# Kernel optimization log

Hardware: AMD Instinct MI355X
Metric: run time of the kernel (lower is better)

The kernel has to match this reference:

```python
import jax, jax.numpy as jnp
import numpy as np
from jax import lax

NUM_TAGS = 54
START = 52
STOP = 53
SEQ_LEN = 512
BATCH = 1024
NEG_INF = -10000.0


def setup_inputs() -> dict:
    key = jax.random.key(0)
    k1, k2, k3 = jax.random.split(key, 3)
    emissions = jax.random.normal(k1, (SEQ_LEN, BATCH, NUM_TAGS), dtype=jnp.float32)
    transitions = jax.random.normal(k2, (NUM_TAGS, NUM_TAGS), dtype=jnp.float32)
    # __init__ clamps: cannot transition TO <start>, cannot transition FROM <stop>
    transitions = transitions.at[START, :].set(NEG_INF)
    transitions = transitions.at[:, STOP].set(NEG_INF)
    tags = jax.random.randint(k3, (SEQ_LEN, BATCH), 0, 52, dtype=jnp.int64)
    mask = jnp.ones((SEQ_LEN, BATCH), dtype=jnp.int32)
    return {"emissions": emissions, "transitions": transitions, "tags": tags, "mask": mask}


def _crf_loss(emissions, transitions, tags, mask):
    S, B, T = emissions.shape
    maskf = mask.astype(emissions.dtype)

    # ---- forward algorithm (log partition), transitions[i, j] = score(j -> i) ----
    alpha0 = jnp.full((B, T), NEG_INF, dtype=emissions.dtype).at[:, START].set(0.0)

    def step(alpha, xs):
        feat, m = xs  # feat: (B, T), m: (B,)
        # (B, T_next, T_prev)
        scores = alpha[:, None, :] + transitions[None, :, :] + feat[:, :, None]
        new_alpha = jax.scipy.special.logsumexp(scores, axis=-1)
        alpha = jnp.where(m[:, None] > 0, new_alpha, alpha)
        return alpha, None

    alpha, _ = lax.scan(step, alpha0, (emissions, maskf))
    alpha = alpha + transitions[STOP][None, :]
    forward_score = jax.scipy.special.logsumexp(alpha, axis=-1)  # (B,)

    # ---- gold score of the given tag sequence ----
    emit = jnp.take_along_axis(emissions, tags[:, :, None], axis=2)[..., 0]  # (S, B)
    trans_t = transitions[tags[1:], tags[:-1]]  # (S-1, B)
    gold = transitions[tags[0], START] + emit[0]
    gold = gold + ((trans_t + emit[1:]) * maskf[1:]).sum(axis=0)
    lengths = mask.sum(axis=0)  # (B,)
    last_tags = tags[lengths - 1, jnp.arange(B)]
    gold = gold + transitions[STOP, last_tags]

    loss = forward_score - gold  # (B,)
    # reduction == 'token_mean'
    return loss.sum() / maskf.sum()


def reference(emissions, transitions, tags, mask):
    return _crf_loss(emissions, transitions, tags, mask)
```

## Files before the change

kernel.cpp:

```cpp
#include <hip/hip_runtime.h>
#include <stdint.h>

#define SEQ    512
#define BATCH  1024
#define NTAG   54
#define TSTART 52
#define TSTOP  53
#define NW     4
#define EMROW  (BATCH * NTAG)


typedef const __attribute__((address_space(1))) void* gld_gptr;
typedef __attribute__((address_space(3))) void*       gld_lptr;

__device__ __forceinline__ void stage4(const float* g, float* l) {
    __builtin_amdgcn_global_load_lds((gld_gptr)g, (gld_lptr)l, 4, 0, 0);
}

#define STEP(o, INC) do {                                                     \
    stage4(gp, (float*)&flds[wv][((o) + 8) & 15][0]);                         \
    gp += (INC);                                                              \
    asm volatile("s_waitcnt vmcnt(8)" ::: "memory");                          \
    float fv_ = flds[wv][(o)][lane];                                          \
    alds[wv][lane] = u;                                                       \
    float efs_ = __expf(fv_) * __uint_as_float((unsigned)(127 - e_lag) << 23);\
    float a0_ = 0.f, a1_ = 0.f, a2_ = 0.f, a3_ = 0.f;                         \
    const float4* ap_ = (const float4*)(&alds[wv][0]);                        \
    _Pragma("unroll")                                                         \
    for (int g_ = 0; g_ < 14; ++g_) {                                         \
        float4 av_ = ap_[g_];                                                 \
        a0_ = fmaf(Elin[4*g_+0], av_.x, a0_);                                 \
        a1_ = fmaf(Elin[4*g_+1], av_.y, a1_);                                 \
        a2_ = fmaf(Elin[4*g_+2], av_.z, a2_);                                 \
        a3_ = fmaf(Elin[4*g_+3], av_.w, a3_);                                 \
    }                                                                         \
    float w_  = (a0_ + a1_) + (a2_ + a3_);                                    \
    float un_ = w_ * efs_;                                                    \
    bool  up_ = (cur & 1ull) != 0ull;                                         \
    cur >>= 1;                                                                \
    u = up_ ? un_ : u;                                                        \
    esum += up_ ? e_lag : 0;                                                  \
    unsigned ub_ = (unsigned)__builtin_amdgcn_readlane(__float_as_int(u), 0); \
    int en_ = (int)((ub_ >> 23) & 255u) - 127;                                \
    e_lag = en_ < -40 ? -40 : (en_ > 40 ? 40 : en_);                          \
} while (0)

__global__ __launch_bounds__(64 * NW, 1) void crf_fwd_kernel(
    const float* __restrict__ em, const float* __restrict__ tr,
    const int* __restrict__ tags, const int* __restrict__ mask,
    float* __restrict__ part, int* __restrict__ msum)
{
    __shared__ float tlds[NTAG * NTAG];
    __shared__ __align__(16) float alds[NW][64];
    __shared__ __align__(16) float flds[NW][16][64];

    const int tid = threadIdx.x;
    for (int k = tid; k < NTAG * NTAG; k += 64 * NW) tlds[k] = tr[k];
    __syncthreads();

    const int wv   = tid >> 6;
    const int lane = tid & 63;
    const int b    = blockIdx.x * NW + wv;
    const size_t bT = (size_t)b * NTAG;

    float Elin[56];
    #pragma unroll
    for (int i = 0; i < 56; ++i) {
        Elin[i] = (lane < NTAG && i < NTAG) ? __expf(tlds[lane * NTAG + i]) : 0.f;
        asm("" : "+v"(Elin[i]));
    }
    float estop = (lane < NTAG) ? __expf(tlds[TSTOP * NTAG + lane]) : 0.f;

    float    goldp = 0.f;
    int      msump = 0;
    uint64_t B[8];
    #pragma unroll
    for (int r = 0; r < 8; ++r) {
        int s  = r * 64 + lane;
        int tg = tags[s * BATCH + b];
        int mk = mask[s * BATCH + b];
        int tp = (s == 0) ? TSTART : tags[(s - 1) * BATCH + b];
        float emv = em[(size_t)s * EMROW + bT + tg];
        float trv = tlds[tg * NTAG + tp];
        float mf  = (s == 0) ? 1.f : (float)mk;
        goldp = fmaf(trv + emv, mf, goldp);
        msump += mk;
        B[r] = __ballot(mk > 0);
    }
    #pragma unroll
    for (int off = 32; off >= 1; off >>= 1) {
        goldp += __shfl_xor(goldp, off);
        msump += __shfl_xor(msump, off);
    }

    float u     = (lane == TSTART) ? 1.f : 0.f;
    int   esum  = 0;
    int   e_lag = 0;

    asm volatile("s_waitcnt vmcnt(0)" ::: "memory");

    const float* gp = em + bT + (lane < NTAG ? lane : NTAG - 1);
    #pragma unroll
    for (int s = 0; s < 8; ++s) {
        stage4(gp, (float*)&flds[wv][s][0]);
        gp += EMROW;
    }

    for (int c = 0; c < 8; ++c) {
        uint64_t cur = B[0];
        for (int q = 0; q < 4; ++q) {
            const size_t incB = (c == 7 && q == 3) ? 0 : (size_t)EMROW;
            STEP( 0, EMROW); STEP( 1, EMROW); STEP( 2, EMROW); STEP( 3, EMROW);
            STEP( 4, EMROW); STEP( 5, EMROW); STEP( 6, EMROW); STEP( 7, incB);
            STEP( 8, incB);  STEP( 9, incB);  STEP(10, incB);  STEP(11, incB);
            STEP(12, incB);  STEP(13, incB);  STEP(14, incB);  STEP(15, incB);
        }
        #pragma unroll
        for (int r = 0; r < 7; ++r) B[r] = B[r + 1];
    }

    float us = u * estop;
    #pragma unroll
    for (int off = 32; off >= 1; off >>= 1) us += __shfl_xor(us, off);
    float fwd = __logf(us) + (float)esum * 0.69314718f;

    asm volatile("s_waitcnt vmcnt(0)" ::: "memory");
    int li   = (msump > 0) ? (msump - 1) : 0;
    int ltag = tags[li * BATCH + b];
    float gold = goldp + tlds[TSTOP * NTAG + ltag];

    if (lane == 0) { part[b] = fwd - gold; msum[b] = msump; }
}

__global__ __launch_bounds__(256) void crf_reduce_kernel(
    const float* __restrict__ part, const int* __restrict__ msum,
    float* __restrict__ out)
{
    const int tid = threadIdx.x;
    float s = 0.f;
    int   m = 0;
    for (int k = tid; k < BATCH; k += 256) { s += part[k]; m += msum[k]; }
    #pragma unroll
    for (int off = 32; off >= 1; off >>= 1) {
        s += __shfl_xor(s, off);
        m += __shfl_xor(m, off);
    }
    __shared__ float sl[4];
    __shared__ int   ml[4];
    if ((tid & 63) == 0) { sl[tid >> 6] = s; ml[tid >> 6] = m; }
    __syncthreads();
    if (tid == 0)
        out[0] = (sl[0] + sl[1] + sl[2] + sl[3]) /
                 (float)(ml[0] + ml[1] + ml[2] + ml[3]);
}

extern "C" void kernel_launch(void* const* d_in, const int* in_sizes, int n_in,
                              void* d_out, int out_size, void* d_ws, size_t ws_size,
                              hipStream_t stream)
{
    const float* em   = (const float*)d_in[0];
    const float* tr   = (const float*)d_in[1];
    const int*   tags = (const int*)d_in[2];
    const int*   mask = (const int*)d_in[3];

    float* part  = (float*)d_ws;
    int*   msumw = (int*)((char*)d_ws + BATCH * sizeof(float));
    float* out   = (float*)d_out;

    crf_fwd_kernel<<<BATCH / NW, 64 * NW, 0, stream>>>(em, tr, tags, mask, part, msumw);
    crf_reduce_kernel<<<1, 256, 0, stream>>>(part, msumw, out);
}
```

Baseline: 167.4 us.

## Pack two batch sequences per wavefront with two tags per lane

Each 64-lane wavefront now handles two batch elements: each half-wave takes one sequence and every lane computes two next-tag outputs, holding two rows of exp-transitions in registers. Blocks become a single wave and the grid doubles to BATCH/2. The aim is to halve the number of serial recurrence chains per wave and keep all lanes busy, where before lanes 54-63 sat idle. The cost is double the register footprint for transitions and more FMAs per step on each lane's critical path, with a risk of spills or lower occupancy.

```diff
diff --git a/kernel.cpp b/kernel.cpp
--- a/kernel.cpp
+++ b/kernel.cpp
@@ -6,7 +6,6 @@
 #define NTAG   54
 #define TSTART 52
 #define TSTOP  53
-#define NW     4
 #define EMROW  (BATCH * NTAG)
 
 
@@ -18,96 +17,126 @@
 }
 
 #define STEP(o, INC) do {                                                     \
-    stage4(gp, (float*)&flds[wv][((o) + 8) & 15][0]);                         \
+    float* sl_ = (float*)&flds[((o) + 8) & 15][0][0];                         \
+    stage4(gp,      sl_);                                                     \
+    stage4(gp + 54, sl_ + 64);                                                \
     gp += (INC);                                                              \
-    asm volatile("s_waitcnt vmcnt(8)" ::: "memory");                          \
-    float fv_ = flds[wv][(o)][lane];                                          \
-    alds[wv][lane] = u;                                                       \
-    float efs_ = __expf(fv_) * __uint_as_float((unsigned)(127 - e_lag) << 23);\
-    float a0_ = 0.f, a1_ = 0.f, a2_ = 0.f, a3_ = 0.f;                         \
-    const float4* ap_ = (const float4*)(&alds[wv][0]);                        \
+    asm volatile("s_waitcnt vmcnt(16)" ::: "memory");                         \
+    *(float2*)&alds[half][rowb] = make_float2(u2x, u2y);                      \
+    float2 fv_ = *(const float2*)&flds[(o)][half][rowb];                      \
+    float sc_  = __uint_as_float((unsigned)(127 - e_lagv) << 23);             \
+    float efx_ = __expf(fv_.x) * sc_;                                         \
+    float efy_ = __expf(fv_.y) * sc_;                                         \
+    float aX0=0.f,aX1=0.f,aX2=0.f,aX3=0.f;                                    \
+    float aY0=0.f,aY1=0.f,aY2=0.f,aY3=0.f;                                    \
+    const float4* up_ = (const float4*)&alds[half][0];                        \
     _Pragma("unroll")                                                         \
     for (int g_ = 0; g_ < 14; ++g_) {                                         \
-        float4 av_ = ap_[g_];                                                 \
-        a0_ = fmaf(Elin[4*g_+0], av_.x, a0_);                                 \
-        a1_ = fmaf(Elin[4*g_+1], av_.y, a1_);                                 \
-        a2_ = fmaf(Elin[4*g_+2], av_.z, a2_);                                 \
-        a3_ = fmaf(Elin[4*g_+3], av_.w, a3_);                                 \
+        float4 uv_ = up_[g_];                                                 \
+        aX0 = fmaf(EX[4*g_+0], uv_.x, aX0);                                   \
+        aY0 = fmaf(EY[4*g_+0], uv_.x, aY0);                                   \
+        aX1 = fmaf(EX[4*g_+1], uv_.y, aX1);                                   \
+        aY1 = fmaf(EY[4*g_+1], uv_.y, aY1);                                   \
+        aX2 = fmaf(EX[4*g_+2], uv_.z, aX2);                                   \
+        aY2 = fmaf(EY[4*g_+2], uv_.z, aY2);                                   \
+        aX3 = fmaf(EX[4*g_+3], uv_.w, aX3);                                   \
+        aY3 = fmaf(EY[4*g_+3], uv_.w, aY3);                                   \
     }                                                                         \
-    float w_  = (a0_ + a1_) + (a2_ + a3_);                                    \
-    float un_ = w_ * efs_;                                                    \
-    bool  up_ = (cur & 1ull) != 0ull;                                         \
-    cur >>= 1;                                                                \
-    u = up_ ? un_ : u;                                                        \
-    esum += up_ ? e_lag : 0;                                                  \
-    unsigned ub_ = (unsigned)__builtin_amdgcn_readlane(__float_as_int(u), 0); \
-    int en_ = (int)((ub_ >> 23) & 255u) - 127;                                \
-    e_lag = en_ < -40 ? -40 : (en_ > 40 ? 40 : en_);                          \
+    float unx_ = ((aX0+aX1)+(aX2+aX3)) * efx_;                                \
+    float uny_ = ((aY0+aY1)+(aY2+aY3)) * efy_;                                \
+    bool upA_ = (curA & 1ull) != 0ull;                                        \
+    bool upB_ = (curB & 1ull) != 0ull;                                        \
+    bool upL_ = (half ? upB_ : upA_) && live;                                 \
+    u2x = upL_ ? unx_ : u2x;                                                  \
+    u2y = upL_ ? uny_ : u2y;                                                  \
+    esum += upL_ ? e_lagv : 0;                                                \
+    curA >>= 1; curB >>= 1;                                                   \
+    int bA_ = __builtin_amdgcn_readlane(__float_as_int(u2x), 0);              \
+    int bB_ = __builtin_amdgcn_readlane(__float_as_int(u2x), 32);             \
+    int eA_ = (((bA_ >> 23) & 255) - 127);                                    \
+    eA_ = eA_ < -40 ? -40 : (eA_ > 40 ? 40 : eA_);                            \
+    int eB_ = (((bB_ >> 23) & 255) - 127);                                    \
+    eB_ = eB_ < -40 ? -40 : (eB_ > 40 ? 40 : eB_);                            \
+    e_lagv = half ? eB_ : eA_;                                                \
 } while (0)
 
-__global__ __launch_bounds__(64 * NW, 1) void crf_fwd_kernel(
+__global__ __launch_bounds__(64, 1) void crf_fwd_kernel(
     const float* __restrict__ em, const float* __restrict__ tr,
     const int* __restrict__ tags, const int* __restrict__ mask,
     float* __restrict__ part, int* __restrict__ msum)
 {
     __shared__ float tlds[NTAG * NTAG];
-    __shared__ __align__(16) float alds[NW][64];
-    __shared__ __align__(16) float flds[NW][16][64];
-
-    const int tid = threadIdx.x;
-    for (int k = tid; k < NTAG * NTAG; k += 64 * NW) tlds[k] = tr[k];
+    __shared__ __align__(16) float alds[2][64];
+    __shared__ __align__(16) float flds[16][2][64];
+
+    const int lane = threadIdx.x;
+    for (int k = lane; k < NTAG * NTAG; k += 64) tlds[k] = tr[k];
     __syncthreads();
 
-    const int wv   = tid >> 6;
-    const int lane = tid & 63;
-    const int b    = blockIdx.x * NW + wv;
-    const size_t bT = (size_t)b * NTAG;
-
-    float Elin[56];
+    const int  b0   = blockIdx.x * 2;
+    const bool half = lane >= 32;
+    const int  l31  = lane & 31;
+    const int  rowb = 2 * l31;
+    const bool live = l31 < 27;
+
+    float EX[56], EY[56];
     #pragma unroll
     for (int i = 0; i < 56; ++i) {
-        Elin[i] = (lane < NTAG && i < NTAG) ? __expf(tlds[lane * NTAG + i]) : 0.f;
-        asm("" : "+v"(Elin[i]));
-    }
-    float estop = (lane < NTAG) ? __expf(tlds[TSTOP * NTAG + lane]) : 0.f;
-
-    float    goldp = 0.f;
-    int      msump = 0;
-    uint64_t B[8];
-    #pragma unroll
-    for (int r = 0; r < 8; ++r) {
-        int s  = r * 64 + lane;
-        int tg = tags[s * BATCH + b];
-        int mk = mask[s * BATCH + b];
-        int tp = (s == 0) ? TSTART : tags[(s - 1) * BATCH + b];
-        float emv = em[(size_t)s * EMROW + bT + tg];
-        float trv = tlds[tg * NTAG + tp];
-        float mf  = (s == 0) ? 1.f : (float)mk;
-        goldp = fmaf(trv + emv, mf, goldp);
-        msump += mk;
-        B[r] = __ballot(mk > 0);
+        EX[i] = (live && i < NTAG) ? __expf(tlds[(rowb    ) * NTAG + i]) : 0.f;
+        EY[i] = (live && i < NTAG) ? __expf(tlds[(rowb + 1) * NTAG + i]) : 0.f;
+        asm("" : "+v"(EX[i]));
+        asm("" : "+v"(EY[i]));
+    }
+    float esx = live ? __expf(tlds[TSTOP * NTAG + rowb    ]) : 0.f;
+    float esy = live ? __expf(tlds[TSTOP * NTAG + rowb + 1]) : 0.f;
+
+    float    gold2[2] = {0.f, 0.f};
+    int      ms2[2]   = {0, 0};
+    uint64_t BA[8], BB[8];
+    #pragma unroll
+    for (int h = 0; h < 2; ++h) {
+        const int b2 = b0 + h;
+        #pragma unroll
+        for (int r = 0; r < 8; ++r) {
+            int s  = r * 64 + lane;
+            int tg = tags[s * BATCH + b2];
+            int mk = mask[s * BATCH + b2];
+            int tp = (s == 0) ? TSTART : tags[(s - 1) * BATCH + b2];
+            float emv = em[(size_t)s * EMROW + (size_t)b2 * NTAG + tg];
+            float trv = tlds[tg * NTAG + tp];
+            float mf  = (s == 0) ? 1.f : (float)mk;
+            gold2[h] = fmaf(trv + emv, mf, gold2[h]);
+            ms2[h] += mk;
+            uint64_t bl = __ballot(mk > 0);
+            if (h == 0) BA[r] = bl; else BB[r] = bl;
+        }
     }
     #pragma unroll
     for (int off = 32; off >= 1; off >>= 1) {
-        goldp += __shfl_xor(goldp, off);
-        msump += __shfl_xor(msump, off);
-    }
-
-    float u     = (lane == TSTART) ? 1.f : 0.f;
-    int   esum  = 0;
-    int   e_lag = 0;
+        gold2[0] += __shfl_xor(gold2[0], off);
+        gold2[1] += __shfl_xor(gold2[1], off);
+        ms2[0]   += __shfl_xor(ms2[0], off);
+        ms2[1]   += __shfl_xor(ms2[1], off);
+    }
+
+    float u2x = (l31 == TSTART / 2) ? 1.f : 0.f;
+    float u2y = 0.f;
+    int   esum   = 0;
+    int   e_lagv = 0;
 
     asm volatile("s_waitcnt vmcnt(0)" ::: "memory");
 
-    const float* gp = em + bT + (lane < NTAG ? lane : NTAG - 1);
+    const float* gp = em + (size_t)b0 * NTAG + (lane < NTAG ? lane : NTAG - 1);
     #pragma unroll
     for (int s = 0; s < 8; ++s) {
-        stage4(gp, (float*)&flds[wv][s][0]);
+        float* sl = (float*)&flds[s][0][0];
+        stage4(gp,      sl);
+        stage4(gp + 54, sl + 64);
         gp += EMROW;
     }
 
     for (int c = 0; c < 8; ++c) {
-        uint64_t cur = B[0];
+        uint64_t curA = BA[0], curB = BB[0];
         for (int q = 0; q < 4; ++q) {
             const size_t incB = (c == 7 && q == 3) ? 0 : (size_t)EMROW;
             STEP( 0, EMROW); STEP( 1, EMROW); STEP( 2, EMROW); STEP( 3, EMROW);
@@ -116,20 +145,23 @@
             STEP(12, incB);  STEP(13, incB);  STEP(14, incB);  STEP(15, incB);
         }
         #pragma unroll
-        for (int r = 0; r < 7; ++r) B[r] = B[r + 1];
-    }
-
-    float us = u * estop;
-    #pragma unroll
-    for (int off = 32; off >= 1; off >>= 1) us += __shfl_xor(us, off);
+        for (int r = 0; r < 7; ++r) { BA[r] = BA[r + 1]; BB[r] = BB[r + 1]; }
+    }
+
+    float us = u2x * esx + u2y * esy;
+    #pragma unroll
+    for (int off = 16; off >= 1; off >>= 1) us += __shfl_xor(us, off);
     float fwd = __logf(us) + (float)esum * 0.69314718f;
 
     asm volatile("s_waitcnt vmcnt(0)" ::: "memory");
-    int li   = (msump > 0) ? (msump - 1) : 0;
-    int ltag = tags[li * BATCH + b];
-    float gold = goldp + tlds[TSTOP * NTAG + ltag];
-
-    if (lane == 0) { part[b] = fwd - gold; msum[b] = msump; }
+    int   myb = half ? b0 + 1 : b0;
+    int   mym = half ? ms2[1] : ms2[0];
+    float myg = half ? gold2[1] : gold2[0];
+    int li    = (mym > 0) ? (mym - 1) : 0;
+    int ltag  = tags[li * BATCH + myb];
+    myg += tlds[TSTOP * NTAG + ltag];
+
+    if (l31 == 0) { part[myb] = fwd - myg; msum[myb] = mym; }
 }
 
 __global__ __launch_bounds__(256) void crf_reduce_kernel(
@@ -167,6 +199,6 @@
     int*   msumw = (int*)((char*)d_ws + BATCH * sizeof(float));
     float* out   = (float*)d_out;
 
-    crf_fwd_kernel<<<BATCH / NW, 64 * NW, 0, stream>>>(em, tr, tags, mask, part, msumw);
+    crf_fwd_kernel<<<BATCH / 2, 64, 0, stream>>>(em, tr, tags, mask, part, msumw);
     crf_reduce_kernel<<<1, 256, 0, stream>>>(part, msumw, out);
 }
```

New measurement: 180.8 us. 8.0% more time.

## Broadcast alpha via readlane and batch emission prefetch with deeper ring

Applied to the files above, without the earlier changes.

The serial forward recurrence no longer round-trips alpha through shared memory each step. Instead it broadcasts each alpha element to scalar registers with readlane and feeds them straight into the FMAs. Emission staging moves to a 32-slot ring with 16 rows in flight. Loads are issued and exponentials computed in groups of 8 steps, which should cut per-step wait and LDS latency. The cost is 54 readlane instructions per step on the critical path, plus extra scalar-register and hazard pressure.

```diff
diff --git a/kernel.cpp b/kernel.cpp
--- a/kernel.cpp
+++ b/kernel.cpp
@@ -17,42 +17,13 @@
     __builtin_amdgcn_global_load_lds((gld_gptr)g, (gld_lptr)l, 4, 0, 0);
 }
 
-#define STEP(o, INC) do {                                                     \
-    stage4(gp, (float*)&flds[wv][((o) + 8) & 15][0]);                         \
-    gp += (INC);                                                              \
-    asm volatile("s_waitcnt vmcnt(8)" ::: "memory");                          \
-    float fv_ = flds[wv][(o)][lane];                                          \
-    alds[wv][lane] = u;                                                       \
-    float efs_ = __expf(fv_) * __uint_as_float((unsigned)(127 - e_lag) << 23);\
-    float a0_ = 0.f, a1_ = 0.f, a2_ = 0.f, a3_ = 0.f;                         \
-    const float4* ap_ = (const float4*)(&alds[wv][0]);                        \
-    _Pragma("unroll")                                                         \
-    for (int g_ = 0; g_ < 14; ++g_) {                                         \
-        float4 av_ = ap_[g_];                                                 \
-        a0_ = fmaf(Elin[4*g_+0], av_.x, a0_);                                 \
-        a1_ = fmaf(Elin[4*g_+1], av_.y, a1_);                                 \
-        a2_ = fmaf(Elin[4*g_+2], av_.z, a2_);                                 \
-        a3_ = fmaf(Elin[4*g_+3], av_.w, a3_);                                 \
-    }                                                                         \
-    float w_  = (a0_ + a1_) + (a2_ + a3_);                                    \
-    float un_ = w_ * efs_;                                                    \
-    bool  up_ = (cur & 1ull) != 0ull;                                         \
-    cur >>= 1;                                                                \
-    u = up_ ? un_ : u;                                                        \
-    esum += up_ ? e_lag : 0;                                                  \
-    unsigned ub_ = (unsigned)__builtin_amdgcn_readlane(__float_as_int(u), 0); \
-    int en_ = (int)((ub_ >> 23) & 255u) - 127;                                \
-    e_lag = en_ < -40 ? -40 : (en_ > 40 ? 40 : en_);                          \
-} while (0)
-
 __global__ __launch_bounds__(64 * NW, 1) void crf_fwd_kernel(
     const float* __restrict__ em, const float* __restrict__ tr,
     const int* __restrict__ tags, const int* __restrict__ mask,
     float* __restrict__ part, int* __restrict__ msum)
 {
     __shared__ float tlds[NTAG * NTAG];
-    __shared__ __align__(16) float alds[NW][64];
-    __shared__ __align__(16) float flds[NW][16][64];
+    __shared__ __align__(16) float flds[NW][32][64];
 
     const int tid = threadIdx.x;
     for (int k = tid; k < NTAG * NTAG; k += 64 * NW) tlds[k] = tr[k];
@@ -63,11 +34,11 @@
     const int b    = blockIdx.x * NW + wv;
     const size_t bT = (size_t)b * NTAG;
 
-    float Elin[56];
+    float E[NTAG];
     #pragma unroll
-    for (int i = 0; i < 56; ++i) {
-        Elin[i] = (lane < NTAG && i < NTAG) ? __expf(tlds[lane * NTAG + i]) : 0.f;
-        asm("" : "+v"(Elin[i]));
+    for (int i = 0; i < NTAG; ++i) {
+        E[i] = (lane < NTAG) ? __expf(tlds[lane * NTAG + i]) : 0.f;
+        asm("" : "+v"(E[i]));
     }
     float estop = (lane < NTAG) ? __expf(tlds[TSTOP * NTAG + lane]) : 0.f;
 
@@ -99,21 +70,52 @@
 
     asm volatile("s_waitcnt vmcnt(0)" ::: "memory");
 
-    const float* gp = em + bT + (lane < NTAG ? lane : NTAG - 1);
+    const float* gbase = em + bT + (lane < NTAG ? lane : NTAG - 1);
     #pragma unroll
-    for (int s = 0; s < 8; ++s) {
-        stage4(gp, (float*)&flds[wv][s][0]);
-        gp += EMROW;
-    }
+    for (int s = 0; s < 16; ++s)
+        stage4(gbase + (size_t)((unsigned)s * (unsigned)EMROW),
+               (float*)&flds[wv][s][0]);
 
-    for (int c = 0; c < 8; ++c) {
+    for (int ch = 0; ch < 8; ++ch) {
         uint64_t cur = B[0];
-        for (int q = 0; q < 4; ++q) {
-            const size_t incB = (c == 7 && q == 3) ? 0 : (size_t)EMROW;
-            STEP( 0, EMROW); STEP( 1, EMROW); STEP( 2, EMROW); STEP( 3, EMROW);
-            STEP( 4, EMROW); STEP( 5, EMROW); STEP( 6, EMROW); STEP( 7, incB);
-            STEP( 8, incB);  STEP( 9, incB);  STEP(10, incB);  STEP(11, incB);
-            STEP(12, incB);  STEP(13, incB);  STEP(14, incB);  STEP(15, incB);
+        #pragma unroll
+        for (int g = 0; g < 8; ++g) {
+            const int gb = ch * 64 + g * 8;
+            asm volatile("s_waitcnt vmcnt(8)" ::: "memory");
+            float ef[8];
+            #pragma unroll
+            for (int k = 0; k < 8; ++k)
+                ef[k] = __expf(flds[wv][(gb + k) & 31][lane]);
+            #pragma unroll
+            for (int k = 0; k < 8; ++k) {
+                int ts = gb + 16 + k;
+                ts = ts > SEQ - 1 ? SEQ - 1 : ts;
+                stage4(gbase + (size_t)((unsigned)ts * (unsigned)EMROW),
+                       (float*)&flds[wv][(gb + 16 + k) & 31][0]);
+            }
+            #pragma unroll
+            for (int k = 0; k < 8; ++k) {
+                int uu = __float_as_int(u);
+                float a0 = 0.f, a1 = 0.f, a2 = 0.f, a3 = 0.f;
+                #pragma unroll
+                for (int i = 0; i < 52; i += 4) {
+                    a0 = fmaf(E[i+0], __int_as_float(__builtin_amdgcn_readlane(uu, i+0)), a0);
+                    a1 = fmaf(E[i+1], __int_as_float(__builtin_amdgcn_readlane(uu, i+1)), a1);
+                    a2 = fmaf(E[i+2], __int_as_float(__builtin_amdgcn_readlane(uu, i+2)), a2);
+                    a3 = fmaf(E[i+3], __int_as_float(__builtin_amdgcn_readlane(uu, i+3)), a3);
+                }
+                a0 = fmaf(E[52], __int_as_float(__builtin_amdgcn_readlane(uu, 52)), a0);
+                a1 = fmaf(E[53], __int_as_float(__builtin_amdgcn_readlane(uu, 53)), a1);
+                float w  = (a0 + a1) + (a2 + a3);
+                float un = w * (ef[k] * __uint_as_float((unsigned)(127 - e_lag) << 23));
+                bool  up = ((cur & 1ull) != 0ull) && (lane < NTAG);
+                u = up ? un : u;
+                esum += up ? e_lag : 0;
+                cur >>= 1;
+                int ub = __builtin_amdgcn_readlane(__float_as_int(u), 0);
+                int en = ((ub >> 23) & 255) - 127;
+                e_lag = en < -40 ? -40 : (en > 40 ? 40 : en);
+            }
         }
         #pragma unroll
         for (int r = 0; r < 7; ++r) B[r] = B[r + 1];
```

Result: faster. 144.5 us (-13.6%).
